# Kernel tuning notes

Hardware: AMD Instinct MI355X
Metric: run time of the kernel (lower is better)

The kernel has to match this reference:

```python
import jax, jax.numpy as jnp
import numpy as np

N = 10000      # nodes
E = 160000     # edges
MUL = 16       # multiplicity of 0e and 1o irreps
NB = 16        # num radial basis
H = 64         # radial MLP hidden
WN = 4 * MUL * MUL  # tensor-product weight_numel (4 CG paths, uvw weights)


def setup_inputs() -> dict:
    key = jax.random.key(0)
    ks = jax.random.split(key, 10)
    node_features = jax.random.normal(ks[0], (N, 4 * MUL), dtype=jnp.float32)  # [N, 16 + 16*3]
    edge_index = jax.random.randint(ks[1], (2, E), 0, N)
    edge_sh = jax.random.normal(ks[2], (E, 4), dtype=jnp.float32)              # 1x0e + 1x1o
    edge_radial_emb = jax.random.uniform(ks[3], (E, NB), dtype=jnp.float32)
    # RadialMLP params
    w1 = jax.random.normal(ks[4], (NB, H), dtype=jnp.float32) / np.sqrt(NB).astype(np.float32)
    b1 = jnp.zeros((H,), jnp.float32)
    w2 = jax.random.normal(ks[5], (H, WN), dtype=jnp.float32) / np.sqrt(H).astype(np.float32)
    b2 = jnp.zeros((WN,), jnp.float32)
    # equivariant Linear params (one [mul,mul] mix per irrep)
    lin_w0 = jax.random.normal(ks[6], (MUL, MUL), dtype=jnp.float32)
    lin_w1 = jax.random.normal(ks[7], (MUL, MUL), dtype=jnp.float32)
    return dict(node_features=node_features, edge_sh=edge_sh, edge_radial_emb=edge_radial_emb,
                w1=w1, b1=b1, w2=w2, b2=b2, lin_w0=lin_w0, lin_w1=lin_w1,
                edge_index=edge_index)


def reference(node_features, edge_sh, edge_radial_emb, w1, b1, w2, b2, lin_w0, lin_w1, edge_index):
    n = node_features.shape[0]
    src, dst = edge_index[0], edge_index[1]
    # radial MLP -> per-edge tensor-product weights, split into the 4 CG paths
    tpw = jax.nn.silu(edge_radial_emb @ w1 + b1) @ w2 + b2        # [E, 4*MUL*MUL]
    W = tpw.reshape(-1, 4, MUL, MUL)
    W00, W01, W10, W11 = W[:, 0], W[:, 1], W[:, 2], W[:, 3]
    # gather source node features, split into scalar (0e) and vector (1o) parts
    xf = node_features[src]
    xs = xf[:, :MUL]                                              # [E, MUL]
    xv = xf[:, MUL:].reshape(-1, MUL, 3)                          # [E, MUL, 3]
    shs = edge_sh[:, 0:1]                                         # [E, 1]
    shv = edge_sh[:, 1:4]                                         # [E, 3]
    alpha = np.float32(1.0 / np.sqrt(2.0 * MUL))  # path norm: 2 paths feed each output irrep
    inv_sqrt3 = np.float32(1.0 / np.sqrt(3.0))    # w3j(1,1,0) contraction constant
    # scalar messages: 0e*0e->0e and 1o*1o->0e
    msg_s = alpha * (jnp.einsum('eu,euv->ev', xs * shs, W00)
                     + inv_sqrt3 * jnp.einsum('eui,ei,euv->ev', xv, shv, W11))
    # vector messages: 0e*1o->1o and 1o*0e->1o
    msg_v = alpha * (jnp.einsum('eu,euv,ei->evi', xs, W01, shv)
                     + jnp.einsum('eui,euv->evi', xv * shs[:, :, None], W10))
    # scatter-sum messages into destination nodes
    agg_s = jax.ops.segment_sum(msg_s, dst, num_segments=n)       # [N, MUL]
    agg_v = jax.ops.segment_sum(msg_v, dst, num_segments=n)       # [N, MUL, 3]
    # equivariant linear (channel mixing per irrep, 1/sqrt(fan_in) norm)
    s = np.float32(1.0 / np.sqrt(MUL))
    ts = (agg_s @ lin_w0) * s
    tv = jnp.einsum('nui,uv->nvi', agg_v, lin_w1) * s
    # NormActivation: x * silu(||x||)/||x||
    eps = np.float32(1e-8)
    ns = jnp.abs(ts)
    act_s = ts * (jax.nn.silu(ns) / (ns + eps))
    nv = jnp.sqrt(jnp.sum(tv * tv, axis=-1))
    act_v = tv * (jax.nn.silu(nv) / (nv + eps))[..., None]
    # identity skip (input irreps == output irreps)
    return node_features + jnp.concatenate([act_s, act_v.reshape(n, MUL * 3)], axis=-1)
```

## Files before the change

kernel.cpp:

```cpp
#include <hip/hip_runtime.h>
#include <hip/hip_bf16.h>
#include <math.h>

#define EPB 64
#define ALPHA 0.17677669529663687f
#define INV_SQRT3 0.57735026918962576f

typedef __attribute__((ext_vector_type(8))) short short8;
typedef __attribute__((ext_vector_type(4))) float f32x4;

__device__ __forceinline__ float silu_f(float x) { return x / (1.0f + __expf(-x)); }

__device__ __forceinline__ unsigned short bf16_rne(float x) {
  unsigned int u = __float_as_uint(x);
  unsigned int r = u + 0x7fffu + ((u >> 16) & 1u);
  return (unsigned short)(r >> 16);
}

__device__ __forceinline__ float bf2f(unsigned short s) {
  return __uint_as_float(((unsigned int)s) << 16);
}

__device__ __forceinline__ void ld4bf(float* d, const unsigned short* s) {
  const uint2 t = *(const uint2*)s;
  d[0] = __uint_as_float(t.x << 16);
  d[1] = __uint_as_float(t.x & 0xffff0000u);
  d[2] = __uint_as_float(t.y << 16);
  d[3] = __uint_as_float(t.y & 0xffff0000u);
}

__global__ __launch_bounds__(256) void prep_kernel(const float* __restrict__ w2,
                                                   unsigned short* __restrict__ w2t,
                                                   const int* __restrict__ eidx,
                                                   int* __restrict__ deg,
                                                   int* __restrict__ rank, int E) {
  if (blockIdx.x < 16) {
    __shared__ unsigned short tile[16][260];
    const int t = threadIdx.x;
    const int k0 = (blockIdx.x & 3) * 16;
    const int c0 = (blockIdx.x >> 2) * 256;
    #pragma unroll
    for (int j = 0; j < 16; ++j)
      tile[j][t] = bf16_rne(w2[(size_t)(k0 + j) * 1024 + c0 + t]);
    __syncthreads();
    union { unsigned short s[16]; uint4 q[2]; } pk;
    #pragma unroll
    for (int j = 0; j < 16; ++j) pk.s[j] = tile[j][t];
    uint4* dst = (uint4*)&w2t[(size_t)(c0 + t) * 64 + k0];
    dst[0] = pk.q[0];
    dst[1] = pk.q[1];
  } else {
    const int e = (blockIdx.x - 16) * 256 + threadIdx.x;
    if (e < E) rank[e] = atomicAdd(&deg[eidx[E + e]], 1);
  }
}

__global__ __launch_bounds__(1024) void scan_kernel(const int* __restrict__ deg,
                                                    int* __restrict__ offs, int N) {
  __shared__ int sums[1024];
  const int t = threadIdx.x;
  const int ch = (N + 1023) >> 10;
  const int lo = t * ch;
  const int hi = min(lo + ch, N);
  int s = 0;
  for (int i = lo; i < hi; ++i) s += deg[i];
  sums[t] = s;
  __syncthreads();
  #pragma unroll
  for (int d = 1; d < 1024; d <<= 1) {
    int v = (t >= d) ? sums[t - d] : 0;
    __syncthreads();
    sums[t] += v;
    __syncthreads();
  }
  int run = sums[t] - s;
  for (int i = lo; i < hi; ++i) { offs[i] = run; run += deg[i]; }
  if (lo < N && hi == N) offs[N] = run;
}

__global__ __launch_bounds__(256, 4) void tfn_edge_kernel(
    const float* __restrict__ nf,
    const float* __restrict__ esh,
    const float* __restrict__ emb,
    const float* __restrict__ w1g,
    const float* __restrict__ b1g,
    const unsigned short* __restrict__ w2t,
    const float* __restrict__ b2g,
    const int*   __restrict__ eidx,
    const int*   __restrict__ rank,
    const int*   __restrict__ offs,
    float* __restrict__ msg,
    float* __restrict__ agg,
    int E, int posmode)
{
  __shared__ __align__(16) unsigned char smem[39168];
  unsigned short* t01  = (unsigned short*)(smem + 0);
  unsigned short* t2s  = (unsigned short*)(smem + 4352);
  unsigned short* t3s  = (unsigned short*)(smem + 6528);
  unsigned short* hsm  = (unsigned short*)(smem + 13056);
  unsigned short* fsT  = (unsigned short*)(smem + 22272);
  unsigned short* fbT  = (unsigned short*)(smem + 24576);
  unsigned short* fxvT = (unsigned short*)(smem + 26880);
  float* b2s   = (float*)(smem + 33792);
  float* shs_l = (float*)(smem + 37888);
  float* shv_l = (float*)(smem + 38144);
  int*   pos_l = (int*)(smem + 38912);
  float* embs = (float*)(smem + 0);
  float* w1s  = (float*)(smem + 4352);

  const int tid = threadIdx.x;
  const int ebase = blockIdx.x * EPB;

  {
    const int e = tid >> 2, p = tid & 3;
    int eg = ebase + e; if (eg >= E) eg = E - 1;

    const float4 em = *(const float4*)&emb[(size_t)eg * 16 + p * 4];
    embs[e * 17 + p * 4 + 0] = em.x;
    embs[e * 17 + p * 4 + 1] = em.y;
    embs[e * 17 + p * 4 + 2] = em.z;
    embs[e * 17 + p * 4 + 3] = em.w;

    const float4 sh = *(const float4*)&esh[(size_t)eg * 4];
    if (p == 0) {
      shs_l[e] = sh.x;
      shv_l[e * 3 + 0] = sh.y; shv_l[e * 3 + 1] = sh.z; shv_l[e * 3 + 2] = sh.w;
      const int dst = eidx[E + eg];
      pos_l[e] = posmode ? (offs[dst] + rank[eg]) : dst;
    }

    const int src = eidx[eg];
    const float4* row4 = (const float4*)(nf + (size_t)src * 64);
    const float4 xs4 = row4[p];
    const float4 va  = row4[4 + p * 3 + 0];
    const float4 vb  = row4[4 + p * 3 + 1];
    const float4 vc  = row4[4 + p * 3 + 2];
    const float xsr[4] = {xs4.x, xs4.y, xs4.z, xs4.w};
    const float xvf[12] = {va.x, va.y, va.z, va.w, vb.x, vb.y, vb.z, vb.w,
                           vc.x, vc.y, vc.z, vc.w};
    #pragma unroll
    for (int uu = 0; uu < 4; ++uu) {
      const int u = p * 4 + uu;
      const float x0 = xvf[uu * 3 + 0];
      const float x1 = xvf[uu * 3 + 1];
      const float x2 = xvf[uu * 3 + 2];
      fsT[u * 72 + e] = bf16_rne(xsr[uu]);
      fbT[u * 72 + e] = bf16_rne(x0 * sh.y + x1 * sh.z + x2 * sh.w);
      fxvT[(0 * 16 + u) * 72 + e] = bf16_rne(x0);
      fxvT[(1 * 16 + u) * 72 + e] = bf16_rne(x1);
      fxvT[(2 * 16 + u) * 72 + e] = bf16_rne(x2);
    }
  }
  {
    const int r = tid >> 4, c4 = (tid & 15) * 4;
    *(float4*)&w1s[r * 64 + c4] = *(const float4*)&w1g[r * 64 + c4];
  }
  *(float4*)&b2s[tid * 4] = *(const float4*)&b2g[tid * 4];
  __syncthreads();

  {
    const int e = tid >> 2, p = tid & 3;
    #pragma unroll
    for (int kk = 0; kk < 16; ++kk) {
      const int c = p * 16 + kk;
      float acc = b1g[c];
      #pragma unroll
      for (int j = 0; j < 16; ++j) acc = fmaf(embs[e * 17 + j], w1s[j * 64 + c], acc);
      hsm[e * 72 + c] = bf16_rne(silu_f(acc));
    }
  }
  __syncthreads();

  const int lane = tid & 63;
  const int sec  = tid >> 6;
  const int q = lane >> 4, m = lane & 15;

  union AF { uint4 u4; short8 s8; };
  AF afr[4][2];
  #pragma unroll
  for (int mt = 0; mt < 4; ++mt)
    #pragma unroll
    for (int ks = 0; ks < 2; ++ks)
      afr[mt][ks].u4 = *(const uint4*)&hsm[(mt * 16 + m) * 72 + ks * 32 + q * 8];

  const unsigned short* ftab = (sec == 3) ? fbT : fsT;
  const uint4* w2tq = (const uint4*)w2t;
  const uint4* bp = w2tq + ((size_t)(sec * 256 + m)) * 8 + q;

  float accA[4][4] = {};
  float accB[4][4] = {};
  float accC[4][4] = {};

  AF b0v, b1v;
  b0v.u4 = bp[0];
  b1v.u4 = bp[4];

  #pragma unroll 2
  for (int u = 0; u < 16; ++u) {
    AF n0, n1;
    if (u < 15) {
      n0.u4 = bp[(u + 1) * 128];
      n1.u4 = bp[(u + 1) * 128 + 4];
    }
    const float b2v = b2s[sec * 256 + u * 16 + m];

    #pragma unroll
    for (int mt = 0; mt < 4; ++mt) {
      f32x4 c = {b2v, b2v, b2v, b2v};
      c = __builtin_amdgcn_mfma_f32_16x16x32_bf16(afr[mt][0].s8, b0v.s8, c, 0, 0, 0);
      c = __builtin_amdgcn_mfma_f32_16x16x32_bf16(afr[mt][1].s8, b1v.s8, c, 0, 0, 0);

      const int fo = mt * 16 + q * 4;
      float fA[4], fB[4], fC[4];
      if (sec == 2) {
        ld4bf(fA, &fxvT[(0 * 16 + u) * 72 + fo]);
        ld4bf(fB, &fxvT[(1 * 16 + u) * 72 + fo]);
        ld4bf(fC, &fxvT[(2 * 16 + u) * 72 + fo]);
        #pragma unroll
        for (int r = 0; r < 4; ++r) {
          accA[mt][r] = fmaf(fA[r], c[r], accA[mt][r]);
          accB[mt][r] = fmaf(fB[r], c[r], accB[mt][r]);
          accC[mt][r] = fmaf(fC[r], c[r], accC[mt][r]);
        }
      } else {
        ld4bf(fA, &ftab[u * 72 + fo]);
        #pragma unroll
        for (int r = 0; r < 4; ++r)
          accA[mt][r] = fmaf(fA[r], c[r], accA[mt][r]);
      }
    }
    if (u < 15) { b0v = n0; b1v = n1; }
  }

  #pragma unroll
  for (int mt = 0; mt < 4; ++mt)
    #pragma unroll
    for (int r = 0; r < 4; ++r) {
      const int e = mt * 16 + q * 4 + r;
      if (sec == 0)      t01[e * 17 + m]        = bf16_rne(accA[mt][r] * shs_l[e]);
      else if (sec == 1) t2s[e * 17 + m]        = bf16_rne(accA[mt][r]);
      else if (sec == 3) t01[1088 + e * 17 + m] = bf16_rne(accA[mt][r]);
      else {
        const float s = shs_l[e];
        t3s[0 * 1088 + e * 17 + m] = bf16_rne(accA[mt][r] * s);
        t3s[1 * 1088 + e * 17 + m] = bf16_rne(accB[mt][r] * s);
        t3s[2 * 1088 + e * 17 + m] = bf16_rne(accC[mt][r] * s);
      }
    }
  __syncthreads();

  {
    const int w = tid >> 6, lc = tid & 63;
    const int cc = lc - 16;
    const int v  = cc / 3;
    const int i3 = cc - v * 3;
    #pragma unroll 1
    for (int t8 = 0; t8 < 16; ++t8) {
      const int e = w * 16 + t8;
      if (ebase + e < E) {
        float val;
        if (lc < 16) {
          val = ALPHA * (bf2f(t01[e * 17 + lc]) + INV_SQRT3 * bf2f(t01[1088 + e * 17 + lc]));
        } else {
          val = ALPHA * (bf2f(t2s[e * 17 + v]) * shv_l[e * 3 + i3] +
                         bf2f(t3s[i3 * 1088 + e * 17 + v]));
        }
        if (posmode) msg[(size_t)pos_l[e] * 64 + lc] = val;
        else         atomicAdd(&agg[(size_t)pos_l[e] * 64 + lc], val);
      }
    }
  }
}

__global__ __launch_bounds__(256) void tfn_agg_node_kernel(
    const float* __restrict__ msg, const int* __restrict__ offs,
    const float* __restrict__ nf, const float* __restrict__ lw0,
    const float* __restrict__ lw1, float* __restrict__ out, int N)
{
  __shared__ float ag[4 * 68];
  __shared__ float w0s[256], w1s[256];
  const int t = threadIdx.x;
  w0s[t] = lw0[t];
  w1s[t] = lw1[t];

  const int n0 = blockIdx.x * 4;
  {
    const int w = t >> 6, lane = t & 63;
    const int n = n0 + w;
    if (n < N) {
      const int s = offs[n], e = offs[n + 1];
      float a0 = 0.0f, a1 = 0.0f, a2 = 0.0f, a3 = 0.0f;
      int j = s;
      for (; j + 3 < e; j += 4) {
        a0 += msg[(size_t)(j + 0) * 64 + lane];
        a1 += msg[(size_t)(j + 1) * 64 + lane];
        a2 += msg[(size_t)(j + 2) * 64 + lane];
        a3 += msg[(size_t)(j + 3) * 64 + lane];
      }
      for (; j < e; ++j) a0 += msg[(size_t)j * 64 + lane];
      ag[w * 68 + lane] = (a0 + a1) + (a2 + a3);
    }
  }
  __syncthreads();
  {
    const int node = t >> 6, c = t & 63;
    const int n = n0 + node;
    if (n >= N) return;
    const float* a = &ag[node * 68];
    float val;
    if (c < 16) {
      float accv = 0.0f;
      #pragma unroll
      for (int u = 0; u < 16; ++u) accv = fmaf(a[u], w0s[u * 16 + c], accv);
      const float ts = 0.25f * accv;
      const float ns = fabsf(ts);
      const float g = (ns / (1.0f + __expf(-ns))) / (ns + 1e-8f);
      val = ts * g;
    } else {
      const int cc = c - 16;
      const int v = cc / 3, i = cc - v * 3;
      float a0 = 0.0f, a1 = 0.0f, a2 = 0.0f;
      #pragma unroll
      for (int u = 0; u < 16; ++u) {
        const float w = w1s[u * 16 + v];
        a0 = fmaf(a[16 + u * 3 + 0], w, a0);
        a1 = fmaf(a[16 + u * 3 + 1], w, a1);
        a2 = fmaf(a[16 + u * 3 + 2], w, a2);
      }
      a0 *= 0.25f; a1 *= 0.25f; a2 *= 0.25f;
      const float nv = sqrtf(a0 * a0 + a1 * a1 + a2 * a2);
      const float g = (nv / (1.0f + __expf(-nv))) / (nv + 1e-8f);
      val = ((i == 0) ? a0 : (i == 1) ? a1 : a2) * g;
    }
    out[(size_t)n * 64 + c] = nf[(size_t)n * 64 + c] + val;
  }
}

__global__ __launch_bounds__(256) void tfn_node_kernel(
    const float* __restrict__ nf,
    const float* __restrict__ lw0,
    const float* __restrict__ lw1,
    float* __restrict__ out, int N)
{
  __shared__ float w0s[256], w1s[256];
  const int tid = threadIdx.x;
  w0s[tid] = lw0[tid];
  w1s[tid] = lw1[tid];
  __syncthreads();

  const int n = blockIdx.x * 256 + tid;
  if (n >= N) return;

  float* rowp = out + (size_t)n * 64;
  float as[16], av[16][3];
  #pragma unroll
  for (int u = 0; u < 16; ++u) as[u] = rowp[u];
  #pragma unroll
  for (int u = 0; u < 16; ++u) {
    av[u][0] = rowp[16 + u * 3 + 0];
    av[u][1] = rowp[16 + u * 3 + 1];
    av[u][2] = rowp[16 + u * 3 + 2];
  }
  const float* nfr = nf + (size_t)n * 64;
  float res[64];

  #pragma unroll
  for (int v = 0; v < 16; ++v) {
    float acc = 0.0f;
    #pragma unroll
    for (int u = 0; u < 16; ++u) acc = fmaf(as[u], w0s[u * 16 + v], acc);
    const float ts = 0.25f * acc;
    const float ns = fabsf(ts);
    const float g = (ns / (1.0f + __expf(-ns))) / (ns + 1e-8f);
    res[v] = nfr[v] + ts * g;
  }
  #pragma unroll
  for (int v = 0; v < 16; ++v) {
    float a0 = 0.0f, a1 = 0.0f, a2 = 0.0f;
    #pragma unroll
    for (int u = 0; u < 16; ++u) {
      const float w = w1s[u * 16 + v];
      a0 = fmaf(av[u][0], w, a0);
      a1 = fmaf(av[u][1], w, a1);
      a2 = fmaf(av[u][2], w, a2);
    }
    a0 *= 0.25f; a1 *= 0.25f; a2 *= 0.25f;
    const float nv = sqrtf(a0 * a0 + a1 * a1 + a2 * a2);
    const float g = (nv / (1.0f + __expf(-nv))) / (nv + 1e-8f);
    res[16 + v * 3 + 0] = nfr[16 + v * 3 + 0] + a0 * g;
    res[16 + v * 3 + 1] = nfr[16 + v * 3 + 1] + a1 * g;
    res[16 + v * 3 + 2] = nfr[16 + v * 3 + 2] + a2 * g;
  }
  #pragma unroll
  for (int o = 0; o < 64; o += 4) {
    *(float4*)&rowp[o] = make_float4(res[o], res[o + 1], res[o + 2], res[o + 3]);
  }
}

extern "C" void kernel_launch(void* const* d_in, const int* in_sizes, int n_in,
                              void* d_out, int out_size, void* d_ws, size_t ws_size,
                              hipStream_t stream) {
  const float* nf  = (const float*)d_in[0];
  const float* esh = (const float*)d_in[1];
  const float* emb = (const float*)d_in[2];
  const float* w1  = (const float*)d_in[3];
  const float* b1  = (const float*)d_in[4];
  const float* w2  = (const float*)d_in[5];
  const float* b2  = (const float*)d_in[6];
  const float* lw0 = (const float*)d_in[7];
  const float* lw1 = (const float*)d_in[8];
  const int*   eix = (const int*)d_in[9];

  const int N = in_sizes[0] / 64;
  const int E = in_sizes[9] / 2;
  float* out = (float*)d_out;

  char* ws = (char*)d_ws;
  const size_t o_w2t  = 0;
  const size_t o_deg  = 131072;
  const size_t o_offs = o_deg  + (((size_t)N * 4 + 15) & ~(size_t)15);
  const size_t o_rank = o_offs + (((size_t)(N + 1) * 4 + 15) & ~(size_t)15);
  const size_t o_msg  = (o_rank + (size_t)E * 4 + 255) & ~(size_t)255;
  const size_t need   = o_msg + (size_t)E * 256;
  const int posmode = (ws_size >= need) ? 1 : 0;

  unsigned short* w2t = (unsigned short*)(ws + o_w2t);
  int*   deg  = (int*)(ws + o_deg);
  int*   offs = (int*)(ws + o_offs);
  int*   rankp = (int*)(ws + o_rank);
  float* msg  = (float*)(ws + o_msg);

  const int eblocks = (E + EPB - 1) / EPB;

  if (posmode) {
    hipMemsetAsync(deg, 0, (size_t)N * 4, stream);
    prep_kernel<<<dim3(16 + (E + 255) / 256), dim3(256), 0, stream>>>(
        w2, w2t, eix, deg, rankp, E);
    scan_kernel<<<dim3(1), dim3(1024), 0, stream>>>(deg, offs, N);
    tfn_edge_kernel<<<dim3(eblocks), dim3(256), 0, stream>>>(
        nf, esh, emb, w1, b1, w2t, b2, eix, rankp, offs, msg, out, E, 1);
    tfn_agg_node_kernel<<<dim3((N + 3) / 4), dim3(256), 0, stream>>>(
        msg, offs, nf, lw0, lw1, out, N);
  } else {
    prep_kernel<<<dim3(16), dim3(256), 0, stream>>>(w2, w2t, eix, nullptr, nullptr, 0);
    hipMemsetAsync(out, 0, (size_t)out_size * sizeof(float), stream);
    tfn_edge_kernel<<<dim3(eblocks), dim3(256), 0, stream>>>(
        nf, esh, emb, w1, b1, w2t, b2, eix, nullptr, nullptr, nullptr, out, E, 0);
    tfn_node_kernel<<<dim3((N + 255) / 256), dim3(256), 0, stream>>>(nf, lw0, lw1, out, N);
  }
}
```

Before: 191.4 us.

## Compute radial MLP first layer with MFMA, keep features in fp32, vectorize aggregation

The first radial-MLP layer, previously scalar FMAs per thread, now runs as a bf16 MFMA from a transposed bf16 copy of w1 and bf16 embeddings. Node-feature tables and intermediate message staging move from bf16 to fp32 in shared memory, with new padding and an extra barrier so the regions can be reused safely. The node aggregation kernel reads float4 rows with four edges in flight per wave and combines them with cross-lane shuffles. The trade is more shared memory per block and a bf16 rounding of the embedding and w1 inputs, in exchange for fewer scalar FMAs and fewer conversions.

```diff
diff --git a/kernel.cpp b/kernel.cpp
--- a/kernel.cpp
+++ b/kernel.cpp
@@ -19,14 +19,6 @@
 
 __device__ __forceinline__ float bf2f(unsigned short s) {
   return __uint_as_float(((unsigned int)s) << 16);
-}
-
-__device__ __forceinline__ void ld4bf(float* d, const unsigned short* s) {
-  const uint2 t = *(const uint2*)s;
-  d[0] = __uint_as_float(t.x << 16);
-  d[1] = __uint_as_float(t.x & 0xffff0000u);
-  d[2] = __uint_as_float(t.y << 16);
-  d[3] = __uint_as_float(t.y & 0xffff0000u);
 }
 
 __global__ __launch_bounds__(256) void prep_kernel(const float* __restrict__ w2,
@@ -93,20 +85,20 @@
     float* __restrict__ agg,
     int E, int posmode)
 {
-  __shared__ __align__(16) unsigned char smem[39168];
-  unsigned short* t01  = (unsigned short*)(smem + 0);
-  unsigned short* t2s  = (unsigned short*)(smem + 4352);
-  unsigned short* t3s  = (unsigned short*)(smem + 6528);
-  unsigned short* hsm  = (unsigned short*)(smem + 13056);
-  unsigned short* fsT  = (unsigned short*)(smem + 22272);
-  unsigned short* fbT  = (unsigned short*)(smem + 24576);
-  unsigned short* fxvT = (unsigned short*)(smem + 26880);
-  float* b2s   = (float*)(smem + 33792);
-  float* shs_l = (float*)(smem + 37888);
-  float* shv_l = (float*)(smem + 38144);
-  int*   pos_l = (int*)(smem + 38912);
-  float* embs = (float*)(smem + 0);
-  float* w1s  = (float*)(smem + 4352);
+  __shared__ __align__(16) unsigned char smem[40288];
+  float* fsT  = (float*)(smem);
+  float* fbT  = (float*)(smem + 4352);
+  float* fxvT = (float*)(smem + 8704);
+  unsigned short* embs = (unsigned short*)(smem + 21760);
+  unsigned short* w1T  = (unsigned short*)(smem + 23808);
+  float* t01 = (float*)(smem);
+  float* t2s = (float*)(smem + 9216);
+  float* t3s = (float*)(smem + 13824);
+  unsigned short* hsm = (unsigned short*)(smem + 27744);
+  unsigned short* b2s = (unsigned short*)(smem + 36960);
+  float* shs_l = (float*)(smem + 39008);
+  float* shv_l = (float*)(smem + 39264);
+  int*   pos_l = (int*)(smem + 40032);
 
   const int tid = threadIdx.x;
   const int ebase = blockIdx.x * EPB;
@@ -116,10 +108,11 @@
     int eg = ebase + e; if (eg >= E) eg = E - 1;
 
     const float4 em = *(const float4*)&emb[(size_t)eg * 16 + p * 4];
-    embs[e * 17 + p * 4 + 0] = em.x;
-    embs[e * 17 + p * 4 + 1] = em.y;
-    embs[e * 17 + p * 4 + 2] = em.z;
-    embs[e * 17 + p * 4 + 3] = em.w;
+    {
+      const unsigned int lo = bf16_rne(em.x) | ((unsigned int)bf16_rne(em.y) << 16);
+      const unsigned int hi = bf16_rne(em.z) | ((unsigned int)bf16_rne(em.w) << 16);
+      *(uint2*)&embs[e * 16 + p * 4] = make_uint2(lo, hi);
+    }
 
     const float4 sh = *(const float4*)&esh[(size_t)eg * 4];
     if (p == 0) {
@@ -144,30 +137,26 @@
       const float x0 = xvf[uu * 3 + 0];
       const float x1 = xvf[uu * 3 + 1];
       const float x2 = xvf[uu * 3 + 2];
-      fsT[u * 72 + e] = bf16_rne(xsr[uu]);
-      fbT[u * 72 + e] = bf16_rne(x0 * sh.y + x1 * sh.z + x2 * sh.w);
-      fxvT[(0 * 16 + u) * 72 + e] = bf16_rne(x0);
-      fxvT[(1 * 16 + u) * 72 + e] = bf16_rne(x1);
-      fxvT[(2 * 16 + u) * 72 + e] = bf16_rne(x2);
+      fsT[u * 68 + e] = xsr[uu];
+      fbT[u * 68 + e] = x0 * sh.y + x1 * sh.z + x2 * sh.w;
+      fxvT[0 * 1088 + u * 68 + e] = x0;
+      fxvT[1 * 1088 + u * 68 + e] = x1;
+      fxvT[2 * 1088 + u * 68 + e] = x2;
     }
   }
   {
     const int r = tid >> 4, c4 = (tid & 15) * 4;
-    *(float4*)&w1s[r * 64 + c4] = *(const float4*)&w1g[r * 64 + c4];
-  }
-  *(float4*)&b2s[tid * 4] = *(const float4*)&b2g[tid * 4];
-  __syncthreads();
-
-  {
-    const int e = tid >> 2, p = tid & 3;
-    #pragma unroll
-    for (int kk = 0; kk < 16; ++kk) {
-      const int c = p * 16 + kk;
-      float acc = b1g[c];
-      #pragma unroll
-      for (int j = 0; j < 16; ++j) acc = fmaf(embs[e * 17 + j], w1s[j * 64 + c], acc);
-      hsm[e * 72 + c] = bf16_rne(silu_f(acc));
-    }
+    const float4 wv = *(const float4*)&w1g[r * 64 + c4];
+    w1T[(c4 + 0) * 16 + r] = bf16_rne(wv.x);
+    w1T[(c4 + 1) * 16 + r] = bf16_rne(wv.y);
+    w1T[(c4 + 2) * 16 + r] = bf16_rne(wv.z);
+    w1T[(c4 + 3) * 16 + r] = bf16_rne(wv.w);
+  }
+  {
+    const float4 bv = *(const float4*)&b2g[tid * 4];
+    const unsigned int lo = bf16_rne(bv.x) | ((unsigned int)bf16_rne(bv.y) << 16);
+    const unsigned int hi = bf16_rne(bv.z) | ((unsigned int)bf16_rne(bv.w) << 16);
+    *(uint2*)&b2s[tid * 4] = make_uint2(lo, hi);
   }
   __syncthreads();
 
@@ -176,6 +165,26 @@
   const int q = lane >> 4, m = lane & 15;
 
   union AF { uint4 u4; short8 s8; };
+
+  {
+    AF ea;
+    if (q < 2) ea.u4 = *(const uint4*)&embs[(sec * 16 + m) * 16 + q * 8];
+    else       ea.u4 = make_uint4(0, 0, 0, 0);
+    #pragma unroll
+    for (int ct = 0; ct < 4; ++ct) {
+      AF wb;
+      if (q < 2) wb.u4 = *(const uint4*)&w1T[(ct * 16 + m) * 16 + q * 8];
+      else       wb.u4 = make_uint4(0, 0, 0, 0);
+      const float b1v = b1g[ct * 16 + m];
+      f32x4 c = {b1v, b1v, b1v, b1v};
+      c = __builtin_amdgcn_mfma_f32_16x16x32_bf16(ea.s8, wb.s8, c, 0, 0, 0);
+      #pragma unroll
+      for (int r = 0; r < 4; ++r)
+        hsm[(sec * 16 + q * 4 + r) * 72 + ct * 16 + m] = bf16_rne(silu_f(c[r]));
+    }
+  }
+  __syncthreads();
+
   AF afr[4][2];
   #pragma unroll
   for (int mt = 0; mt < 4; ++mt)
@@ -183,7 +192,7 @@
     for (int ks = 0; ks < 2; ++ks)
       afr[mt][ks].u4 = *(const uint4*)&hsm[(mt * 16 + m) * 72 + ks * 32 + q * 8];
 
-  const unsigned short* ftab = (sec == 3) ? fbT : fsT;
+  const float* ftab = (sec == 3) ? fbT : fsT;
   const uint4* w2tq = (const uint4*)w2t;
   const uint4* bp = w2tq + ((size_t)(sec * 256 + m)) * 8 + q;
 
@@ -202,7 +211,7 @@
       n0.u4 = bp[(u + 1) * 128];
       n1.u4 = bp[(u + 1) * 128 + 4];
     }
-    const float b2v = b2s[sec * 256 + u * 16 + m];
+    const float b2v = bf2f(b2s[sec * 256 + u * 16 + m]);
 
     #pragma unroll
     for (int mt = 0; mt < 4; ++mt) {
@@ -211,11 +220,13 @@
       c = __builtin_amdgcn_mfma_f32_16x16x32_bf16(afr[mt][1].s8, b1v.s8, c, 0, 0, 0);
 
       const int fo = mt * 16 + q * 4;
-      float fA[4], fB[4], fC[4];
       if (sec == 2) {
-        ld4bf(fA, &fxvT[(0 * 16 + u) * 72 + fo]);
-        ld4bf(fB, &fxvT[(1 * 16 + u) * 72 + fo]);
-        ld4bf(fC, &fxvT[(2 * 16 + u) * 72 + fo]);
+        const float4 f0 = *(const float4*)&fxvT[0 * 1088 + u * 68 + fo];
+        const float4 f1 = *(const float4*)&fxvT[1 * 1088 + u * 68 + fo];
+        const float4 f2 = *(const float4*)&fxvT[2 * 1088 + u * 68 + fo];
+        const float fA[4] = {f0.x, f0.y, f0.z, f0.w};
+        const float fB[4] = {f1.x, f1.y, f1.z, f1.w};
+        const float fC[4] = {f2.x, f2.y, f2.z, f2.w};
         #pragma unroll
         for (int r = 0; r < 4; ++r) {
           accA[mt][r] = fmaf(fA[r], c[r], accA[mt][r]);
@@ -223,7 +234,8 @@
           accC[mt][r] = fmaf(fC[r], c[r], accC[mt][r]);
         }
       } else {
-        ld4bf(fA, &ftab[u * 72 + fo]);
+        const float4 f = *(const float4*)&ftab[u * 68 + fo];
+        const float fA[4] = {f.x, f.y, f.z, f.w};
         #pragma unroll
         for (int r = 0; r < 4; ++r)
           accA[mt][r] = fmaf(fA[r], c[r], accA[mt][r]);
@@ -232,19 +244,21 @@
     if (u < 15) { b0v = n0; b1v = n1; }
   }
 
+  __syncthreads();
+
   #pragma unroll
   for (int mt = 0; mt < 4; ++mt)
     #pragma unroll
     for (int r = 0; r < 4; ++r) {
       const int e = mt * 16 + q * 4 + r;
-      if (sec == 0)      t01[e * 17 + m]        = bf16_rne(accA[mt][r] * shs_l[e]);
-      else if (sec == 1) t2s[e * 17 + m]        = bf16_rne(accA[mt][r]);
-      else if (sec == 3) t01[1088 + e * 17 + m] = bf16_rne(accA[mt][r]);
+      if (sec == 0)      t01[e * 18 + m]        = accA[mt][r] * shs_l[e];
+      else if (sec == 1) t2s[e * 18 + m]        = accA[mt][r];
+      else if (sec == 3) t01[1152 + e * 18 + m] = accA[mt][r];
       else {
         const float s = shs_l[e];
-        t3s[0 * 1088 + e * 17 + m] = bf16_rne(accA[mt][r] * s);
-        t3s[1 * 1088 + e * 17 + m] = bf16_rne(accB[mt][r] * s);
-        t3s[2 * 1088 + e * 17 + m] = bf16_rne(accC[mt][r] * s);
+        t3s[0 * 1160 + e * 18 + m] = accA[mt][r] * s;
+        t3s[1 * 1160 + e * 18 + m] = accB[mt][r] * s;
+        t3s[2 * 1160 + e * 18 + m] = accC[mt][r] * s;
       }
     }
   __syncthreads();
@@ -260,10 +274,9 @@
       if (ebase + e < E) {
         float val;
         if (lc < 16) {
-          val = ALPHA * (bf2f(t01[e * 17 + lc]) + INV_SQRT3 * bf2f(t01[1088 + e * 17 + lc]));
+          val = ALPHA * (t01[e * 18 + lc] + INV_SQRT3 * t01[1152 + e * 18 + lc]);
         } else {
-          val = ALPHA * (bf2f(t2s[e * 17 + v]) * shv_l[e * 3 + i3] +
-                         bf2f(t3s[i3 * 1088 + e * 17 + v]));
+          val = ALPHA * (t2s[e * 18 + v] * shv_l[e * 3 + i3] + t3s[i3 * 1160 + e * 18 + v]);
         }
         if (posmode) msg[(size_t)pos_l[e] * 64 + lc] = val;
         else         atomicAdd(&agg[(size_t)pos_l[e] * 64 + lc], val);
@@ -286,19 +299,20 @@
   const int n0 = blockIdx.x * 4;
   {
     const int w = t >> 6, lane = t & 63;
+    const int rq = lane >> 4, cl = lane & 15;
     const int n = n0 + w;
     if (n < N) {
       const int s = offs[n], e = offs[n + 1];
       float a0 = 0.0f, a1 = 0.0f, a2 = 0.0f, a3 = 0.0f;
-      int j = s;
-      for (; j + 3 < e; j += 4) {
-        a0 += msg[(size_t)(j + 0) * 64 + lane];
-        a1 += msg[(size_t)(j + 1) * 64 + lane];
-        a2 += msg[(size_t)(j + 2) * 64 + lane];
-        a3 += msg[(size_t)(j + 3) * 64 + lane];
+      for (int j = s + rq; j < e; j += 4) {
+        const float4 v = *(const float4*)&msg[(size_t)j * 64 + cl * 4];
+        a0 += v.x; a1 += v.y; a2 += v.z; a3 += v.w;
       }
-      for (; j < e; ++j) a0 += msg[(size_t)j * 64 + lane];
-      ag[w * 68 + lane] = (a0 + a1) + (a2 + a3);
+      a0 += __shfl_xor(a0, 16); a0 += __shfl_xor(a0, 32);
+      a1 += __shfl_xor(a1, 16); a1 += __shfl_xor(a1, 32);
+      a2 += __shfl_xor(a2, 16); a2 += __shfl_xor(a2, 32);
+      a3 += __shfl_xor(a3, 16); a3 += __shfl_xor(a3, 32);
+      if (rq == 0) *(float4*)&ag[w * 68 + cl * 4] = make_float4(a0, a1, a2, a3);
     }
   }
   __syncthreads();
```

New measurement: 224.7 us. +17.4%, slower.
